# Kernel tuning notes

Measured on AMD Instinct MI355X. Metric: run time of the kernel, lower is better.

The kernel has to match this reference:

```python
import jax, jax.numpy as jnp
import numpy as np

INF = 1e20
NEG_FILL = -9e15  # value used by the torch module for masked entries
ALPHA = 0.2       # LeakyReLU negative slope
N, DIN, DOUT = 8192, 512, 512
EDGE_P = 0.1


def setup_inputs() -> dict:
    key = jax.random.key(0)
    k1, k2, k3, k4, k5 = jax.random.split(key, 5)
    inp = jax.random.normal(k1, (N, DIN), dtype=jnp.float32)
    # adjacency: 0.0 where an edge exists, -INF (non-edge) elsewhere
    u = jax.random.uniform(k2, (N, N), dtype=jnp.float32)
    adj = jnp.where(u < EDGE_P, 0.0, jnp.float32(-INF))
    # xavier_uniform with gain=1.414
    def xavier(k, shape, gain=1.414):
        fan_in, fan_out = shape[0], shape[1]
        bound = gain * np.sqrt(6.0 / (fan_in + fan_out))
        return jax.random.uniform(k, shape, dtype=jnp.float32, minval=-bound, maxval=bound)
    W = xavier(k3, (DIN, DOUT))
    a1 = xavier(k4, (DOUT, 1))
    a2 = xavier(k5, (DOUT, 1))
    return {"input": inp, "adj": adj, "W": W, "a1": a1, "a2": a2}


def reference(input, adj, W, a1, a2):
    h = input @ W                       # [N, DOUT]
    e1 = h @ a1                         # [N, 1] source score
    e2 = h @ a2                         # [N, 1] target score
    e = jax.nn.leaky_relu(e1 + e2.T, negative_slope=ALPHA)  # [N, N] additive score
    att = jnp.where(adj != -INF, e, jnp.float32(NEG_FILL))  # mask non-edges
    att = jax.nn.softmax(att, axis=-1)
    h_prime = att @ h                   # [N, DOUT]
    return jnp.tanh(h_prime)            # concat=True branch
```

## Files before the change

### kernel.cpp

```cpp
#include <hip/hip_runtime.h>
#include <stdint.h>

#define NN 8192
#define DD 512
#define SPLIT 4
#define ITERS_PER_SPLIT 16

typedef uint16_t u16;
typedef __bf16 bf16x8_t __attribute__((ext_vector_type(8)));
typedef float f32x4_t __attribute__((ext_vector_type(4)));
typedef uint32_t u32x4_t __attribute__((ext_vector_type(4)));

__device__ __forceinline__ u16 f2bf(float x) {
  uint32_t u = __builtin_bit_cast(uint32_t, x);
  u += 0x7FFFu + ((u >> 16) & 1u);
  return (u16)(u >> 16);
}
__device__ __forceinline__ float h2f(uint32_t bits) {
  return (float)__builtin_bit_cast(_Float16, (u16)bits);
}

__device__ __forceinline__ unsigned encf(float f) {
  unsigned u = __builtin_bit_cast(unsigned, f);
  return (u & 0x80000000u) ? ~u : (u | 0x80000000u);
}
__device__ __forceinline__ float decf(unsigned e) {
  unsigned u = (e & 0x80000000u) ? (e & 0x7FFFFFFFu) : ~e;
  return __builtin_bit_cast(float, u);
}

__global__ __launch_bounds__(256) void k_convert_W(const float* __restrict__ W,
                                                   u16* __restrict__ WT,
                                                   unsigned* __restrict__ maxenc) {
  int t = blockIdx.x * blockDim.x + threadIdx.x;
  if (t == 0) *maxenc = 0u;
  int n = t >> 6;
  int k8 = (t & 63) << 3;
  u16 tmp[8];
#pragma unroll
  for (int j = 0; j < 8; ++j) tmp[j] = f2bf(W[(size_t)(k8 + j) * DD + n]);
  uint32_t w0 = (uint32_t)tmp[0] | ((uint32_t)tmp[1] << 16);
  uint32_t w1 = (uint32_t)tmp[2] | ((uint32_t)tmp[3] << 16);
  uint32_t w2 = (uint32_t)tmp[4] | ((uint32_t)tmp[5] << 16);
  uint32_t w3 = (uint32_t)tmp[6] | ((uint32_t)tmp[7] << 16);
  *(uint4*)&WT[(size_t)n * DD + k8] = make_uint4(w0, w1, w2, w3);
}

__global__ __launch_bounds__(256) void k_gemm_h(const float* __restrict__ Af,
                                                const u16* __restrict__ BT,
                                                u16* __restrict__ HT,
                                                const float* __restrict__ a1,
                                                const float* __restrict__ a2,
                                                float* __restrict__ e1part,
                                                float* __restrict__ e2part) {
  __shared__ __align__(16) u16 As[128 * 32];
  __shared__ __align__(16) u16 Bs[128 * 32];
  const int tid = threadIdx.x;
  const int wid = tid >> 6, lane = tid & 63;
  const int wr = wid >> 1, wc = wid & 1;
  const int lr = lane & 15, kg = lane >> 4;
  const int rowBase = blockIdx.x * 128;
  const int colBase = blockIdx.y * 128;
  const int sr = tid >> 2, sc = tid & 3;
  f32x4_t acc[4][4] = {};
  for (int kt = 0; kt < 16; ++kt) {
    const int k0 = kt * 32 + sc * 8;
    {
      float4 f0 = *(const float4*)&Af[(size_t)(rowBase + sr) * DD + k0];
      float4 f1 = *(const float4*)&Af[(size_t)(rowBase + sr) * DD + k0 + 4];
      *(uint4*)&As[tid * 8] = make_uint4(
          (uint32_t)f2bf(f0.x) | ((uint32_t)f2bf(f0.y) << 16),
          (uint32_t)f2bf(f0.z) | ((uint32_t)f2bf(f0.w) << 16),
          (uint32_t)f2bf(f1.x) | ((uint32_t)f2bf(f1.y) << 16),
          (uint32_t)f2bf(f1.z) | ((uint32_t)f2bf(f1.w) << 16));
      float4 g0 = *(const float4*)&Af[(size_t)(rowBase + 64 + sr) * DD + k0];
      float4 g1 = *(const float4*)&Af[(size_t)(rowBase + 64 + sr) * DD + k0 + 4];
      *(uint4*)&As[(tid + 256) * 8] = make_uint4(
          (uint32_t)f2bf(g0.x) | ((uint32_t)f2bf(g0.y) << 16),
          (uint32_t)f2bf(g0.z) | ((uint32_t)f2bf(g0.w) << 16),
          (uint32_t)f2bf(g1.x) | ((uint32_t)f2bf(g1.y) << 16),
          (uint32_t)f2bf(g1.z) | ((uint32_t)f2bf(g1.w) << 16));
    }
    *(uint4*)&Bs[tid * 8] = *(const uint4*)&BT[(size_t)(colBase + sr) * DD + k0];
    *(uint4*)&Bs[(tid + 256) * 8] = *(const uint4*)&BT[(size_t)(colBase + 64 + sr) * DD + k0];
    __syncthreads();
    bf16x8_t af[4], bfv[4];
#pragma unroll
    for (int mt = 0; mt < 4; ++mt)
      af[mt] = *(const bf16x8_t*)&As[(wr * 64 + mt * 16 + lr) * 32 + kg * 8];
#pragma unroll
    for (int nt = 0; nt < 4; ++nt)
      bfv[nt] = *(const bf16x8_t*)&Bs[(wc * 64 + nt * 16 + lr) * 32 + kg * 8];
#pragma unroll
    for (int mt = 0; mt < 4; ++mt)
#pragma unroll
      for (int nt = 0; nt < 4; ++nt)
        acc[mt][nt] = __builtin_amdgcn_mfma_f32_16x16x32_bf16(af[mt], bfv[nt], acc[mt][nt], 0, 0, 0);
    __syncthreads();
  }
  float a1v[4], a2v[4];
#pragma unroll
  for (int nt = 0; nt < 4; ++nt) {
    const int col = colBase + wc * 64 + nt * 16 + lr;
    a1v[nt] = a1[col];
    a2v[nt] = a2[col];
  }
  const int cg = blockIdx.y * 2 + wc;
#pragma unroll
  for (int mt = 0; mt < 4; ++mt) {
#pragma unroll
    for (int nt = 0; nt < 4; ++nt) {
      const int row0 = rowBase + wr * 64 + mt * 16 + kg * 4;
      const int col = colBase + wc * 64 + nt * 16 + lr;
      uint32_t lo = (uint32_t)f2bf(acc[mt][nt][0]) | ((uint32_t)f2bf(acc[mt][nt][1]) << 16);
      uint32_t hi = (uint32_t)f2bf(acc[mt][nt][2]) | ((uint32_t)f2bf(acc[mt][nt][3]) << 16);
      *(uint2*)&HT[(size_t)col * NN + row0] = make_uint2(lo, hi);
    }
#pragma unroll
    for (int r = 0; r < 4; ++r) {
      float t1 = 0.f, t2 = 0.f;
#pragma unroll
      for (int nt = 0; nt < 4; ++nt) {
        t1 += acc[mt][nt][r] * a1v[nt];
        t2 += acc[mt][nt][r] * a2v[nt];
      }
#pragma unroll
      for (int m = 1; m <= 8; m <<= 1) {
        t1 += __shfl_xor(t1, m);
        t2 += __shfl_xor(t2, m);
      }
      if (lr == 0) {
        const int row = rowBase + wr * 64 + mt * 16 + kg * 4 + r;
        e1part[(size_t)cg * NN + row] = t1;
        e2part[(size_t)cg * NN + row] = t2;
      }
    }
  }
}

__global__ __launch_bounds__(256) void k_e12small(const float* __restrict__ e1part,
                                                  const float* __restrict__ e2part,
                                                  float* __restrict__ e1, float* __restrict__ e2,
                                                  unsigned* __restrict__ maxenc) {
  const int row = blockIdx.x * 256 + threadIdx.x;
  float s1 = 0.f, s2 = 0.f;
#pragma unroll
  for (int cg = 0; cg < 8; ++cg) {
    s1 += e1part[(size_t)cg * NN + row];
    s2 += e2part[(size_t)cg * NN + row];
  }
  e1[row] = s1;
  e2[row] = s2;
  atomicMax(maxenc, encf(s2));
}

__global__ __launch_bounds__(1024) void k_fused(const float* __restrict__ adj,
                                                const u16* __restrict__ HT,
                                                const float* __restrict__ e1,
                                                const float* __restrict__ e2,
                                                const unsigned* __restrict__ maxenc,
                                                u16* __restrict__ numpart,
                                                float* __restrict__ denpart) {
  __shared__ __align__(16) u16 P[2][128 * 128];
  __shared__ __align__(16) float e2s[256 * 12];
  __shared__ float partsum[2048];
  const int tid = threadIdx.x;
  const int wid = tid >> 6;
  const int lane = tid & 63;
  const int lr = lane & 15;
  const int kg = lane >> 4;
  const int b = blockIdx.x;
  const int xcd = b & 7;
  const int bz = xcd >> 1;
  const int rowBlock = (b >> 3) + ((xcd & 1) << 5);
  const int rowBase = rowBlock * 128;
  const int kk0 = bz * ITERS_PER_SPLIT;
  const int c = (tid >> 4) & 15;
  const int m = tid & 15;
  const int mt0 = tid >> 8;
  const int r0l = mt0 * 16 + m;
  const float e1r0 = e1[rowBase + r0l];
  const float e1r1 = e1[rowBase + r0l + 64];
  const float mE2 = decf(*maxenc);
  const float xb0 = e1r0 + mE2, xb1 = e1r1 + mE2;
  const float bnd0 = fmaxf(xb0, 0.2f * xb0);
  const float bnd1 = fmaxf(xb1, 0.2f * xb1);
  {
    const float* e2g = e2 + kk0 * 128;
    if (tid < 256) {
      float4 u0 = *(const float4*)(e2g + tid * 8);
      float4 u1 = *(const float4*)(e2g + tid * 8 + 4);
      *(float4*)&e2s[tid * 12] = u0;
      *(float4*)&e2s[tid * 12 + 4] = u1;
    }
  }
  const float* adjp0 = adj + (size_t)(rowBase + r0l) * NN + c * 8;
  const float* adjp1 = adjp0 + (size_t)64 * NN;
  const int n0 = wid * 32;
  const u16* btp0 = HT + (size_t)(n0 + 0 + lr) * NN + kg * 8;
  const u16* btp1 = HT + (size_t)(n0 + 16 + lr) * NN + kg * 8;
  float dsum0 = 0.f, dsum1 = 0.f;
  f32x4_t acc[8][2] = {};
  f32x4_t a00 = __builtin_nontemporal_load((const f32x4_t*)(adjp0 + kk0 * 128));
  f32x4_t a01 = __builtin_nontemporal_load((const f32x4_t*)(adjp0 + kk0 * 128 + 4));
  f32x4_t a10 = __builtin_nontemporal_load((const f32x4_t*)(adjp1 + kk0 * 128));
  f32x4_t a11 = __builtin_nontemporal_load((const f32x4_t*)(adjp1 + kk0 * 128 + 4));
  __syncthreads();
  for (int t = 0; t < ITERS_PER_SPLIT; ++t) {
    const int colBase = (kk0 + t) * 128;
    const float* eg = &e2s[(t * 16 + c) * 12];
    f32x4_t ev0 = *(const f32x4_t*)eg;
    f32x4_t ev1 = *(const f32x4_t*)(eg + 4);
    float ee[8] = {ev0[0], ev0[1], ev0[2], ev0[3], ev1[0], ev1[1], ev1[2], ev1[3]};
    float aa0[8] = {a00[0], a00[1], a00[2], a00[3], a01[0], a01[1], a01[2], a01[3]};
    float aa1[8] = {a10[0], a10[1], a10[2], a10[3], a11[0], a11[1], a11[2], a11[3]};
    float pv0[8], pv1[8];
#pragma unroll
    for (int j = 0; j < 8; ++j) {
      float x0 = e1r0 + ee[j];
      float s0 = fmaxf(x0, 0.2f * x0);
      float p0 = (aa0[j] > -1e19f) ? __expf(s0 - bnd0) : 0.f;
      pv0[j] = p0;
      dsum0 += p0;
      float x1 = e1r1 + ee[j];
      float s1 = fmaxf(x1, 0.2f * x1);
      float p1 = (aa1[j] > -1e19f) ? __expf(s1 - bnd1) : 0.f;
      pv1[j] = p1;
      dsum1 += p1;
    }
    {
      uint32_t w0 = (uint32_t)f2bf(pv0[0]) | ((uint32_t)f2bf(pv0[1]) << 16);
      uint32_t w1 = (uint32_t)f2bf(pv0[2]) | ((uint32_t)f2bf(pv0[3]) << 16);
      uint32_t w2 = (uint32_t)f2bf(pv0[4]) | ((uint32_t)f2bf(pv0[5]) << 16);
      uint32_t w3 = (uint32_t)f2bf(pv0[6]) | ((uint32_t)f2bf(pv0[7]) << 16);
      *(uint4*)&P[t & 1][tid * 8] = make_uint4(w0, w1, w2, w3);
      uint32_t v0 = (uint32_t)f2bf(pv1[0]) | ((uint32_t)f2bf(pv1[1]) << 16);
      uint32_t v1 = (uint32_t)f2bf(pv1[2]) | ((uint32_t)f2bf(pv1[3]) << 16);
      uint32_t v2 = (uint32_t)f2bf(pv1[4]) | ((uint32_t)f2bf(pv1[5]) << 16);
      uint32_t v3 = (uint32_t)f2bf(pv1[6]) | ((uint32_t)f2bf(pv1[7]) << 16);
      *(uint4*)&P[t & 1][(tid + 1024) * 8] = make_uint4(v0, v1, v2, v3);
    }
    if (t + 1 < ITERS_PER_SPLIT) {
      const float* q0 = adjp0 + colBase + 128;
      const float* q1 = adjp1 + colBase + 128;
      a00 = __builtin_nontemporal_load((const f32x4_t*)q0);
      a01 = __builtin_nontemporal_load((const f32x4_t*)(q0 + 4));
      a10 = __builtin_nontemporal_load((const f32x4_t*)q1);
      a11 = __builtin_nontemporal_load((const f32x4_t*)(q1 + 4));
    }
    bf16x8_t bc0 = *(const bf16x8_t*)(btp0 + colBase);
    bf16x8_t bc1 = *(const bf16x8_t*)(btp1 + colBase);
    asm volatile("s_waitcnt lgkmcnt(0)" ::: "memory");
    __builtin_amdgcn_s_barrier();
    const u16* pb = &P[t & 1][0];
#pragma unroll
    for (int ks = 0; ks < 4; ++ks) {
      bf16x8_t bn0, bn1;
      if (ks < 3) {
        const int co = colBase + (ks + 1) * 32;
        bn0 = *(const bf16x8_t*)(btp0 + co);
        bn1 = *(const bf16x8_t*)(btp1 + co);
      }
#pragma unroll
      for (int mt = 0; mt < 8; ++mt) {
        bf16x8_t af = *(const bf16x8_t*)(pb + mt * 2048 + ks * 512 + lane * 8);
        acc[mt][0] = __builtin_amdgcn_mfma_f32_16x16x32_bf16(af, bc0, acc[mt][0], 0, 0, 0);
        acc[mt][1] = __builtin_amdgcn_mfma_f32_16x16x32_bf16(af, bc1, acc[mt][1], 0, 0, 0);
      }
      if (ks < 3) { bc0 = bn0; bc1 = bn1; }
    }
  }
  partsum[tid] = dsum0;
  partsum[tid + 1024] = dsum1;
  __syncthreads();
  if (tid < 128) {
    const int rr = tid;
    const int rlo = rr & 63;
    const int off = (rr >> 6) << 10;
    float s = 0.f;
#pragma unroll
    for (int cc = 0; cc < 16; ++cc)
      s += partsum[off + (rlo >> 4) * 256 + cc * 16 + (rlo & 15)];
    denpart[(size_t)bz * NN + rowBase + rr] = s;
  }
  u16* np = numpart + (size_t)bz * NN * DD;
#pragma unroll
  for (int mt = 0; mt < 8; ++mt)
#pragma unroll
    for (int nt = 0; nt < 2; ++nt)
#pragma unroll
      for (int r = 0; r < 4; ++r) {
        const int rowL = mt * 16 + kg * 4 + r;
        _Float16 hv = (_Float16)acc[mt][nt][r];
        __builtin_nontemporal_store(__builtin_bit_cast(u16, hv),
                                    &np[(size_t)(rowBase + rowL) * DD + n0 + nt * 16 + lr]);
      }
}

__global__ __launch_bounds__(256) void k_combine(const u16* __restrict__ num,
                                                 const float* __restrict__ den,
                                                 float* __restrict__ out) {
  const size_t idx = (size_t)blockIdx.x * 256 + threadIdx.x;
  const int row = (int)(idx >> 6);
  float d = den[row] + den[NN + row] + den[2 * NN + row] + den[3 * NN + row];
  const u32x4_t* nv = (const u32x4_t*)num;
  const size_t stride = (size_t)NN * DD / 8;
  float s[8] = {};
#pragma unroll
  for (int sl = 0; sl < 4; ++sl) {
    u32x4_t q = __builtin_nontemporal_load(nv + sl * stride + idx);
    s[0] += h2f(q[0] & 0xffff); s[1] += h2f(q[0] >> 16);
    s[2] += h2f(q[1] & 0xffff); s[3] += h2f(q[1] >> 16);
    s[4] += h2f(q[2] & 0xffff); s[5] += h2f(q[2] >> 16);
    s[6] += h2f(q[3] & 0xffff); s[7] += h2f(q[3] >> 16);
  }
  const float inv = (d > 0.f) ? 1.f / d : 0.f;
  f32x4_t o0, o1;
#pragma unroll
  for (int j = 0; j < 4; ++j) o0[j] = 1.f - 2.f / (__expf(2.f * (s[j] * inv)) + 1.f);
#pragma unroll
  for (int j = 0; j < 4; ++j) o1[j] = 1.f - 2.f / (__expf(2.f * (s[4 + j] * inv)) + 1.f);
  __builtin_nontemporal_store(o0, ((f32x4_t*)out) + idx * 2);
  __builtin_nontemporal_store(o1, ((f32x4_t*)out) + idx * 2 + 1);
}

extern "C" void kernel_launch(void* const* d_in, const int* in_sizes, int n_in,
                              void* d_out, int out_size, void* d_ws, size_t ws_size,
                              hipStream_t stream) {
  const float* input = (const float*)d_in[0];
  const float* adj   = (const float*)d_in[1];
  const float* W     = (const float*)d_in[2];
  const float* a1    = (const float*)d_in[3];
  const float* a2    = (const float*)d_in[4];
  float* out = (float*)d_out;
  char* ws = (char*)d_ws;

  u16* hT        = (u16*)ws;
  float* e1      = (float*)(ws + 8388608);
  float* e2      = (float*)(ws + 8421376);
  unsigned* mx   = (unsigned*)(ws + 8454144);
  float* denp    = (float*)(ws + 8454400);
  float* e1p     = (float*)(ws + 8585472);
  float* e2p     = (float*)(ws + 8847616);
  u16* nump      = (u16*)(ws + 9109760);
  u16* WT        = (u16*)(ws + 9109760);

  hipLaunchKernelGGL(k_convert_W, dim3(128), dim3(256), 0, stream, W, WT, mx);
  hipLaunchKernelGGL(k_gemm_h, dim3(64, 4), dim3(256), 0, stream, input, WT, hT, a1, a2, e1p, e2p);
  hipLaunchKernelGGL(k_e12small, dim3(32), dim3(256), 0, stream, e1p, e2p, e1, e2, mx);
  hipLaunchKernelGGL(k_fused, dim3(64 * SPLIT), dim3(1024), 0, stream, adj, hT, e1, e2, mx, nump, denp);
  hipLaunchKernelGGL(k_combine, dim3(2048), dim3(256), 0, stream, nump, denp, out);
}
```

Baseline: 177.8 us.

## Software-pipeline softmax P-slab build for next tile under current MFMA chunks

Builds the bf16 exp probability slab for iteration t+1 in the other P buffer while the MFMA k-chunks of iteration t run, with a prologue that builds slab 0. The aim is to hide the VALU exp/convert work behind matrix-core work and cut the per-iteration barrier bubble from two phases to one. It keeps one barrier per iteration but raises register pressure, since adj loads, B fragments and accumulators are all live at once.

```diff
diff --git a/kernel.cpp b/kernel.cpp
--- a/kernel.cpp
+++ b/kernel.cpp
@@ -206,41 +206,49 @@
   f32x4_t a10 = __builtin_nontemporal_load((const f32x4_t*)(adjp1 + kk0 * 128));
   f32x4_t a11 = __builtin_nontemporal_load((const f32x4_t*)(adjp1 + kk0 * 128 + 4));
   __syncthreads();
+
+#define BUILD_SLAB(tt, qb, SL)                                                              \
+  {                                                                                         \
+    const float* eg_ = &e2s[((tt) * 16 + c) * 12];                                          \
+    f32x4_t ev0_ = *(const f32x4_t*)eg_;                                                    \
+    f32x4_t ev1_ = *(const f32x4_t*)(eg_ + 4);                                              \
+    float ee_[8] = {ev0_[0], ev0_[1], ev0_[2], ev0_[3], ev1_[0], ev1_[1], ev1_[2], ev1_[3]};\
+    float aa_[8];                                                                           \
+    if (SL) { aa_[0]=a10[0];aa_[1]=a10[1];aa_[2]=a10[2];aa_[3]=a10[3];                      \
+              aa_[4]=a11[0];aa_[5]=a11[1];aa_[6]=a11[2];aa_[7]=a11[3]; }                    \
+    else    { aa_[0]=a00[0];aa_[1]=a00[1];aa_[2]=a00[2];aa_[3]=a00[3];                      \
+              aa_[4]=a01[0];aa_[5]=a01[1];aa_[6]=a01[2];aa_[7]=a01[3]; }                    \
+    const float e1r_ = SL ? e1r1 : e1r0;                                                    \
+    const float bnd_ = SL ? bnd1 : bnd0;                                                    \
+    float pv_[8];                                                                           \
+    _Pragma("unroll")                                                                       \
+    for (int j = 0; j < 8; ++j) {                                                           \
+      float x_ = e1r_ + ee_[j];                                                             \
+      float s_ = fmaxf(x_, 0.2f * x_);                                                      \
+      float p_ = (aa_[j] > -1e19f) ? __expf(s_ - bnd_) : 0.f;                               \
+      pv_[j] = p_;                                                                          \
+      if (SL) dsum1 += p_; else dsum0 += p_;                                                \
+    }                                                                                       \
+    uint32_t w0_ = (uint32_t)f2bf(pv_[0]) | ((uint32_t)f2bf(pv_[1]) << 16);                 \
+    uint32_t w1_ = (uint32_t)f2bf(pv_[2]) | ((uint32_t)f2bf(pv_[3]) << 16);                 \
+    uint32_t w2_ = (uint32_t)f2bf(pv_[4]) | ((uint32_t)f2bf(pv_[5]) << 16);                 \
+    uint32_t w3_ = (uint32_t)f2bf(pv_[6]) | ((uint32_t)f2bf(pv_[7]) << 16);                 \
+    *(uint4*)&(qb)[(tid + (SL ? 1024 : 0)) * 8] = make_uint4(w0_, w1_, w2_, w3_);           \
+  }
+
+  BUILD_SLAB(0, P[0], 0)
+  BUILD_SLAB(0, P[0], 1)
+  bf16x8_t bc0 = *(const bf16x8_t*)(btp0 + kk0 * 128);
+  bf16x8_t bc1 = *(const bf16x8_t*)(btp1 + kk0 * 128);
+  asm volatile("s_waitcnt lgkmcnt(0)" ::: "memory");
+  __builtin_amdgcn_s_barrier();
+
   for (int t = 0; t < ITERS_PER_SPLIT; ++t) {
     const int colBase = (kk0 + t) * 128;
-    const float* eg = &e2s[(t * 16 + c) * 12];
-    f32x4_t ev0 = *(const f32x4_t*)eg;
-    f32x4_t ev1 = *(const f32x4_t*)(eg + 4);
-    float ee[8] = {ev0[0], ev0[1], ev0[2], ev0[3], ev1[0], ev1[1], ev1[2], ev1[3]};
-    float aa0[8] = {a00[0], a00[1], a00[2], a00[3], a01[0], a01[1], a01[2], a01[3]};
-    float aa1[8] = {a10[0], a10[1], a10[2], a10[3], a11[0], a11[1], a11[2], a11[3]};
-    float pv0[8], pv1[8];
-#pragma unroll
-    for (int j = 0; j < 8; ++j) {
-      float x0 = e1r0 + ee[j];
-      float s0 = fmaxf(x0, 0.2f * x0);
-      float p0 = (aa0[j] > -1e19f) ? __expf(s0 - bnd0) : 0.f;
-      pv0[j] = p0;
-      dsum0 += p0;
-      float x1 = e1r1 + ee[j];
-      float s1 = fmaxf(x1, 0.2f * x1);
-      float p1 = (aa1[j] > -1e19f) ? __expf(s1 - bnd1) : 0.f;
-      pv1[j] = p1;
-      dsum1 += p1;
-    }
-    {
-      uint32_t w0 = (uint32_t)f2bf(pv0[0]) | ((uint32_t)f2bf(pv0[1]) << 16);
-      uint32_t w1 = (uint32_t)f2bf(pv0[2]) | ((uint32_t)f2bf(pv0[3]) << 16);
-      uint32_t w2 = (uint32_t)f2bf(pv0[4]) | ((uint32_t)f2bf(pv0[5]) << 16);
-      uint32_t w3 = (uint32_t)f2bf(pv0[6]) | ((uint32_t)f2bf(pv0[7]) << 16);
-      *(uint4*)&P[t & 1][tid * 8] = make_uint4(w0, w1, w2, w3);
-      uint32_t v0 = (uint32_t)f2bf(pv1[0]) | ((uint32_t)f2bf(pv1[1]) << 16);
-      uint32_t v1 = (uint32_t)f2bf(pv1[2]) | ((uint32_t)f2bf(pv1[3]) << 16);
-      uint32_t v2 = (uint32_t)f2bf(pv1[4]) | ((uint32_t)f2bf(pv1[5]) << 16);
-      uint32_t v3 = (uint32_t)f2bf(pv1[6]) | ((uint32_t)f2bf(pv1[7]) << 16);
-      *(uint4*)&P[t & 1][(tid + 1024) * 8] = make_uint4(v0, v1, v2, v3);
-    }
-    if (t + 1 < ITERS_PER_SPLIT) {
+    const u16* pb = &P[t & 1][0];
+    u16* qb = &P[(t + 1) & 1][0];
+    const bool more = (t + 1 < ITERS_PER_SPLIT);
+    if (more) {
       const float* q0 = adjp0 + colBase + 128;
       const float* q1 = adjp1 + colBase + 128;
       a00 = __builtin_nontemporal_load((const f32x4_t*)q0);
@@ -248,28 +256,50 @@
       a10 = __builtin_nontemporal_load((const f32x4_t*)q1);
       a11 = __builtin_nontemporal_load((const f32x4_t*)(q1 + 4));
     }
-    bf16x8_t bc0 = *(const bf16x8_t*)(btp0 + colBase);
-    bf16x8_t bc1 = *(const bf16x8_t*)(btp1 + colBase);
+    bf16x8_t bn0, bn1;
+    bn0 = *(const bf16x8_t*)(btp0 + colBase + 32);
+    bn1 = *(const bf16x8_t*)(btp1 + colBase + 32);
+#pragma unroll
+    for (int mt = 0; mt < 8; ++mt) {
+      bf16x8_t af = *(const bf16x8_t*)(pb + mt * 2048 + 0 * 512 + lane * 8);
+      acc[mt][0] = __builtin_amdgcn_mfma_f32_16x16x32_bf16(af, bc0, acc[mt][0], 0, 0, 0);
+      acc[mt][1] = __builtin_amdgcn_mfma_f32_16x16x32_bf16(af, bc1, acc[mt][1], 0, 0, 0);
+    }
+    bc0 = bn0; bc1 = bn1;
+    if (more) BUILD_SLAB(t + 1, qb, 0)
+    bn0 = *(const bf16x8_t*)(btp0 + colBase + 64);
+    bn1 = *(const bf16x8_t*)(btp1 + colBase + 64);
+#pragma unroll
+    for (int mt = 0; mt < 8; ++mt) {
+      bf16x8_t af = *(const bf16x8_t*)(pb + mt * 2048 + 1 * 512 + lane * 8);
+      acc[mt][0] = __builtin_amdgcn_mfma_f32_16x16x32_bf16(af, bc0, acc[mt][0], 0, 0, 0);
+      acc[mt][1] = __builtin_amdgcn_mfma_f32_16x16x32_bf16(af, bc1, acc[mt][1], 0, 0, 0);
+    }
+    bc0 = bn0; bc1 = bn1;
+    if (more) BUILD_SLAB(t + 1, qb, 1)
+    bn0 = *(const bf16x8_t*)(btp0 + colBase + 96);
+    bn1 = *(const bf16x8_t*)(btp1 + colBase + 96);
+#pragma unroll
+    for (int mt = 0; mt < 8; ++mt) {
+      bf16x8_t af = *(const bf16x8_t*)(pb + mt * 2048 + 2 * 512 + lane * 8);
+      acc[mt][0] = __builtin_amdgcn_mfma_f32_16x16x32_bf16(af, bc0, acc[mt][0], 0, 0, 0);
+      acc[mt][1] = __builtin_amdgcn_mfma_f32_16x16x32_bf16(af, bc1, acc[mt][1], 0, 0, 0);
+    }
+    bc0 = bn0; bc1 = bn1;
+#pragma unroll
+    for (int mt = 0; mt < 8; ++mt) {
+      bf16x8_t af = *(const bf16x8_t*)(pb + mt * 2048 + 3 * 512 + lane * 8);
+      acc[mt][0] = __builtin_amdgcn_mfma_f32_16x16x32_bf16(af, bc0, acc[mt][0], 0, 0, 0);
+      acc[mt][1] = __builtin_amdgcn_mfma_f32_16x16x32_bf16(af, bc1, acc[mt][1], 0, 0, 0);
+    }
+    if (more) {
+      bc0 = *(const bf16x8_t*)(btp0 + colBase + 128);
+      bc1 = *(const bf16x8_t*)(btp1 + colBase + 128);
+    }
     asm volatile("s_waitcnt lgkmcnt(0)" ::: "memory");
     __builtin_amdgcn_s_barrier();
-    const u16* pb = &P[t & 1][0];
-#pragma unroll
-    for (int ks = 0; ks < 4; ++ks) {
-      bf16x8_t bn0, bn1;
-      if (ks < 3) {
-        const int co = colBase + (ks + 1) * 32;
-        bn0 = *(const bf16x8_t*)(btp0 + co);
-        bn1 = *(const bf16x8_t*)(btp1 + co);
-      }
-#pragma unroll
-      for (int mt = 0; mt < 8; ++mt) {
-        bf16x8_t af = *(const bf16x8_t*)(pb + mt * 2048 + ks * 512 + lane * 8);
-        acc[mt][0] = __builtin_amdgcn_mfma_f32_16x16x32_bf16(af, bc0, acc[mt][0], 0, 0, 0);
-        acc[mt][1] = __builtin_amdgcn_mfma_f32_16x16x32_bf16(af, bc1, acc[mt][1], 0, 0, 0);
-      }
-      if (ks < 3) { bc0 = bn0; bc1 = bn1; }
-    }
-  }
+  }
+#undef BUILD_SLAB
   partsum[tid] = dsum0;
   partsum[tid + 1024] = dsum1;
   __syncthreads();
```

After: 227.1 us. 1.28x slower.
